# Kernel tuning notes

Measured on AMD Instinct MI355X. Metric: run time of the kernel, lower is better.

## Reference

```python
import jax, jax.numpy as jnp
import numpy as np
from jax import lax

DIM = 512
DH = 16          # dim_head
H = DIM // DH    # 32 heads
WS = 7           # window_size
SR = 3           # sr_ratio (AvgPool2d kernel, stride=1)
EPS = 1e-5


def _rel_pos_indices():
    # mirrors the torch buffer construction, incl. the [:, 24:] slice for sr_ratio>1
    pos = np.arange(WS)
    gi, gj = np.meshgrid(pos, pos, indexing='ij')
    grid = np.stack([gi, gj], axis=-1).reshape(-1, 2)            # (49, 2)
    rel = grid[:, None, :] - grid[None, :, :] + (WS - 1)         # (49, 49, 2)
    idx = rel[..., 0] * (2 * WS - 1) + rel[..., 1]               # (49, 49)
    return jnp.asarray(idx[:, 24:], dtype=jnp.int32)             # (49, 25)


def _layernorm(x, g, b):
    m = jnp.mean(x, axis=-1, keepdims=True)
    v = jnp.mean(jnp.square(x - m), axis=-1, keepdims=True)
    return (x - m) * lax.rsqrt(v + EPS) * g + b


def setup_inputs() -> dict:
    key = jax.random.key(0)
    ks = jax.random.split(key, 8)
    B, X, Y = 8, 14, 14
    x = jax.random.normal(ks[0], (B, X, Y, WS, WS, DIM), dtype=jnp.float32)
    ln_gamma = 1.0 + 0.1 * jax.random.normal(ks[1], (DIM,), dtype=jnp.float32)
    ln_beta = 0.1 * jax.random.normal(ks[2], (DIM,), dtype=jnp.float32)
    s = 1.0 / np.sqrt(DIM)
    Wq = jax.random.normal(ks[3], (DIM, DIM), dtype=jnp.float32) * s
    Wkv = jax.random.normal(ks[4], (2 * DIM, DIM), dtype=jnp.float32) * s
    Wout = jax.random.normal(ks[5], (DIM, DIM), dtype=jnp.float32) * s
    rel_pos_emb = 0.02 * jax.random.normal(ks[6], ((2 * WS - 1) ** 2, H), dtype=jnp.float32)
    return {"x": x, "ln_gamma": ln_gamma, "ln_beta": ln_beta,
            "Wq": Wq, "Wkv": Wkv, "Wout": Wout, "rel_pos_emb": rel_pos_emb}


def reference(x, ln_gamma, ln_beta, Wq, Wkv, Wout, rel_pos_emb):
    B, X, Y, W1, W2, D = x.shape
    Nw = B * X * Y                      # number of windows
    Nq = W1 * W2                        # 49 query tokens per window
    xn = _layernorm(x, ln_gamma, ln_beta)
    xw = xn.reshape(Nw, Nq, D)
    # queries
    q = (xw @ Wq.T).reshape(Nw, Nq, H, DH).transpose(0, 2, 1, 3) * (DH ** -0.5)  # (Nw,H,Nq,DH)
    # KV spatial reduction: AvgPool2d(kernel=SR, stride=1) over the 7x7 window
    xi = xw.reshape(Nw, W1, W2, D)
    xp = lax.reduce_window(xi, 0.0, lax.add, (1, SR, SR, 1), (1, 1, 1, 1), 'VALID') / (SR * SR)
    Hp, Wp = W1 - SR + 1, W2 - SR + 1   # 5, 5
    xkv = _layernorm(xp.reshape(Nw, Hp * Wp, D), ln_gamma, ln_beta)
    # to_kv with einops '(dim h l)' decomposition: last axis factored as (DH, H, 2)
    kv = (xkv @ Wkv.T).reshape(Nw, Hp * Wp, DH, H, 2)
    k = kv[..., 0].transpose(0, 3, 1, 2)  # (Nw, H, Nk, DH)
    v = kv[..., 1].transpose(0, 3, 1, 2)
    sim = jnp.einsum('bhid,bhjd->bhij', q, k)                    # (Nw,H,49,25)
    bias = rel_pos_emb[_rel_pos_indices()]                       # (49,25,H)
    sim = sim + bias.transpose(2, 0, 1)[None]
    attn = jax.nn.softmax(sim, axis=-1)
    out = jnp.einsum('bhij,bhjd->bhid', attn, v)                 # (Nw,H,49,DH)
    out = out.reshape(Nw, H, W1, W2, DH).transpose(0, 2, 3, 1, 4).reshape(Nw, W1, W2, D)
    out = out @ Wout.T
    return out.reshape(B, X, Y, W1, W2, D)
```

## Files before the change

kernel.cpp:

```cpp
#include <hip/hip_runtime.h>

typedef _Float16 half8 __attribute__((ext_vector_type(8)));
typedef float f32x4 __attribute__((ext_vector_type(4)));

#define MFMA16(a,b,c) __builtin_amdgcn_mfma_f32_16x16x32_f16(a,b,c,0,0,0)
#define GLOAD16(g, l) __builtin_amdgcn_global_load_lds( \
  (const __attribute__((address_space(1))) void*)(g), \
  (__attribute__((address_space(3))) void*)(l), 16, 0, 0)

static constexpr int NW     = 1568;
static constexpr int MROWSQ = 76832;
static constexpr int MPADQ  = 76928;
static constexpr int MROWKV = 39200;
static constexpr int MPADKV = 39296;

__device__ __forceinline__ half8 h8z(){
  half8 z = {(_Float16)0,(_Float16)0,(_Float16)0,(_Float16)0,
             (_Float16)0,(_Float16)0,(_Float16)0,(_Float16)0};
  return z;
}

__global__ void k_prep_w(const float* __restrict__ a, const float* __restrict__ b,
                         const float* __restrict__ c,
                         _Float16* __restrict__ ah, _Float16* __restrict__ bh,
                         _Float16* __restrict__ ch){
  int i = blockIdx.x*256 + threadIdx.x;
  if(i < 262144) ah[i] = (_Float16)(a[i]*0.25f);
  int j = i - 262144;
  if(j >= 0 && j < 524288) bh[j] = (_Float16)b[j];
  int k = i - 786432;
  if(k >= 0 && k < 262144) ch[k] = (_Float16)c[k];
}

__global__ void k_prep_bias(const float* __restrict__ rel, float* __restrict__ biasT){
  int t = blockIdx.x*256 + threadIdx.x;
  if(t >= 65536) return;
  int h = t >> 11;
  int r = t & 2047;
  int i = r >> 5, slotk = r & 31;
  int kg = slotk >> 3, idx = slotk & 7;
  int j = (idx < 4) ? (kg*4 + idx) : (16 + kg*4 + idx - 4);
  float v = 0.f;
  if(j >= 25) v = -1e30f;
  else if(i < 49){
    int qi = i/7, qj = i%7;
    int c = j + 24, ki = c/7, kj = c%7;
    v = rel[((qi-ki+6)*13 + (qj-kj+6))*32 + h];
  }
  biasT[t] = v;
}

__global__ __launch_bounds__(512) void k_ln_pool(const float* __restrict__ x,
    const float* __restrict__ gamma, const float* __restrict__ beta,
    _Float16* __restrict__ xn, _Float16* __restrict__ xkv){
  __shared__ _Float16 nrm[49*512];
  const int w = blockIdx.x, t = threadIdx.x;
  const int lane = t & 63, wv = t >> 6;
  float gf[8], bf[8];
  {
    float4 g0 = *(const float4*)(gamma + lane*8);
    float4 g1 = *(const float4*)(gamma + lane*8 + 4);
    float4 b0 = *(const float4*)(beta  + lane*8);
    float4 b1 = *(const float4*)(beta  + lane*8 + 4);
    gf[0]=g0.x; gf[1]=g0.y; gf[2]=g0.z; gf[3]=g0.w;
    gf[4]=g1.x; gf[5]=g1.y; gf[6]=g1.z; gf[7]=g1.w;
    bf[0]=b0.x; bf[1]=b0.y; bf[2]=b0.z; bf[3]=b0.w;
    bf[4]=b1.x; bf[5]=b1.y; bf[6]=b1.z; bf[7]=b1.w;
  }
  const float* xw = x + (size_t)w*49*512;
  for(int i = wv; i < 49; i += 8){
    const float* row = xw + i*512 + lane*8;
    float4 v0 = *(const float4*)row;
    float4 v1 = *(const float4*)(row+4);
    float v[8] = {v0.x,v0.y,v0.z,v0.w,v1.x,v1.y,v1.z,v1.w};
    float s = 0.f, sq = 0.f;
    #pragma unroll
    for(int j=0;j<8;j++){ s += v[j]; sq += v[j]*v[j]; }
    #pragma unroll
    for(int o=32;o>=1;o>>=1){ s += __shfl_xor(s,o); sq += __shfl_xor(sq,o); }
    float mean = s*(1.f/512.f);
    float rstd = rsqrtf(sq*(1.f/512.f) - mean*mean + 1e-5f);
    half8 nh;
    #pragma unroll
    for(int j=0;j<8;j++)
      nh[j] = (_Float16)((v[j]-mean)*rstd*gf[j] + bf[j]);
    *(half8*)&nrm[i*512 + lane*8] = nh;
    *(half8*)(xn + ((size_t)w*49 + i)*512 + lane*8) = nh;
  }
  __syncthreads();
  for(int p = wv; p < 25; p += 8){
    const int pi = p/5, pj = p%5;
    float acc[8] = {0,0,0,0,0,0,0,0};
    #pragma unroll
    for(int a=0;a<3;a++)
      #pragma unroll
      for(int bb=0;bb<3;bb++){
        half8 rv = *(const half8*)&nrm[((pi+a)*7 + (pj+bb))*512 + lane*8];
        #pragma unroll
        for(int j=0;j<8;j++) acc[j] += (float)rv[j];
      }
    float s = 0.f, sq = 0.f;
    #pragma unroll
    for(int j=0;j<8;j++){ acc[j] *= (1.f/9.f); s += acc[j]; sq += acc[j]*acc[j]; }
    #pragma unroll
    for(int o=32;o>=1;o>>=1){ s += __shfl_xor(s,o); sq += __shfl_xor(sq,o); }
    float mean = s*(1.f/512.f);
    float rstd = rsqrtf(sq*(1.f/512.f) - mean*mean + 1e-5f);
    half8 nh;
    #pragma unroll
    for(int j=0;j<8;j++) nh[j] = (_Float16)((acc[j]-mean)*rstd*gf[j] + bf[j]);
    *(half8*)(xkv + ((size_t)w*25 + p)*512 + lane*8) = nh;
  }
}

template<int MODE>
__global__ __launch_bounds__(256) void k_gemm(const _Float16* __restrict__ A,
    const _Float16* __restrict__ Bw, _Float16* __restrict__ oh,
    float* __restrict__ of, int ldc){
  __shared__ __align__(16) _Float16 As[128*32];
  __shared__ __align__(16) _Float16 Bs[128*32];
  const int m0 = blockIdx.y*128, n0 = blockIdx.x*128;
  const int t = threadIdx.x, lane = t & 63;
  const int wid = t >> 6, wm = (wid>>1)*64, wn = (wid&1)*64;
  const int lr = lane & 15, kg = lane >> 4;
  f32x4 acc[4][4] = {};
  const _Float16* Ab = A  + (size_t)m0*512;
  const _Float16* Bb = Bw + (size_t)n0*512;
  for(int k0 = 0; k0 < 512; k0 += 32){
    #pragma unroll
    for(int c=0;c<2;c++){
      int foff = c*256 + wid*64;
      int f = foff + lane;
      const _Float16* sa = Ab + (size_t)(f>>2)*512 + k0 + (f&3)*8;
      const _Float16* sb = Bb + (size_t)(f>>2)*512 + k0 + (f&3)*8;
      GLOAD16(sa, As + foff*8);
      GLOAD16(sb, Bs + foff*8);
    }
    __syncthreads();
    half8 af[4], bf[4];
    #pragma unroll
    for(int mt=0;mt<4;mt++) af[mt] = *(const half8*)&As[(wm + mt*16 + lr)*32 + kg*8];
    #pragma unroll
    for(int nt=0;nt<4;nt++) bf[nt] = *(const half8*)&Bs[(wn + nt*16 + lr)*32 + kg*8];
    #pragma unroll
    for(int mt=0;mt<4;mt++)
      #pragma unroll
      for(int nt=0;nt<4;nt++)
        acc[mt][nt] = MFMA16(af[mt], bf[nt], acc[mt][nt]);
    __syncthreads();
  }
  #pragma unroll
  for(int mt=0;mt<4;mt++)
    #pragma unroll
    for(int nt=0;nt<4;nt++)
      #pragma unroll
      for(int r=0;r<4;r++){
        int row = m0 + wm + mt*16 + kg*4 + r;
        int col = n0 + wn + nt*16 + lr;
        float vv = acc[mt][nt][r];
        if(MODE == 0){
          oh[(size_t)row*ldc + col] = (_Float16)vv;
        } else {
          if(row < MROWSQ) of[(size_t)row*ldc + col] = vv;
        }
      }
}

__global__ __launch_bounds__(256) void k_repack(const _Float16* __restrict__ kvb,
    _Float16* __restrict__ kb, _Float16* __restrict__ vb){
  __shared__ uint2 s2[6400];
  uint32_t* su = (uint32_t*)s2;
  const int w = blockIdx.x, t = threadIdx.x;
  const uint2* src = (const uint2*)(kvb + (size_t)w*25*1024);
  #pragma unroll
  for(int it=0; it<25; ++it){
    int U = it*256 + t;
    int j = U >> 8, u = U & 255;
    s2[j*256 + (u ^ (u>>4) ^ (j&15))] = src[U];
  }
  __syncthreads();
  _Float16* kdst = kb + (size_t)w*12800;
  _Float16* vdst = vb + (size_t)w*12800;
  for(int it=0; it<7; ++it){
    int q = it*256 + t;
    if(q < 1600){
      int h = q/50, rem = q%50, j = rem>>1, half = rem&1;
      half8 k8, v8;
      #pragma unroll
      for(int jj=0;jj<8;jj++){
        int dh = half*8 + jj;
        int slot = j*256 + ((dh*16 + (h>>1)) ^ dh ^ (j&15));
        uint32_t val = su[slot*2 + (h&1)];
        k8[jj] = ((_Float16*)&val)[0];
        v8[jj] = ((_Float16*)&val)[1];
      }
      *(half8*)(kdst + q*8) = k8;
      *(half8*)(vdst + q*8) = v8;
    }
  }
}

__global__ __launch_bounds__(256) void k_attn(const _Float16* __restrict__ q,
    const _Float16* __restrict__ kb, const _Float16* __restrict__ vb,
    const float* __restrict__ biasT, _Float16* __restrict__ ao){
  const int w = blockIdx.x, hi = blockIdx.y, t = threadIdx.x;
  const int lane = t & 63, wv = t >> 6;
  const int lr = lane & 15, kg = lane >> 4;
  const size_t qbase = ((size_t)w*49)*512;
  const int hA = hi*4 + wv;
  const size_t kvA = (((size_t)w*32 + hA)*25)*16;
  const size_t kvB = kvA + 6400;
  half8 kA0=h8z(), kA1=h8z(), kB0=h8z(), kB1=h8z();
  if(kg < 2){
    kA0 = *(const half8*)(kb + kvA + lr*16 + kg*8);
    kB0 = *(const half8*)(kb + kvB + lr*16 + kg*8);
    if(lr < 9){
      kA1 = *(const half8*)(kb + kvA + (16+lr)*16 + kg*8);
      kB1 = *(const half8*)(kb + kvB + (16+lr)*16 + kg*8);
    }
  }
  half8 qA[4], qB[4];
  #pragma unroll
  for(int qt=0;qt<4;qt++){
    if(kg < 2){
      const _Float16* p = q + qbase + (size_t)(qt*16+lr)*512 + hA*16 + kg*8;
      qA[qt] = *(const half8*)p;
      qB[qt] = *(const half8*)(p + 256);
    } else { qA[qt] = h8z(); qB[qt] = h8z(); }
  }
  half8 vA = h8z(), vB = h8z();
  #pragma unroll
  for(int idx=0; idx<8; idx++){
    int key = (idx<4) ? (kg*4+idx) : (16 + kg*4 + idx-4);
    if(key < 25){
      vA[idx] = vb[kvA + key*16 + lr];
      vB[idx] = vb[kvB + key*16 + lr];
    }
  }
  const float4* btA = (const float4*)(biasT + (size_t)hA*2048);
  const float4* btB = (const float4*)(biasT + (size_t)(hA+16)*2048);
  #pragma unroll
  for(int qt=0;qt<4;qt++){
    f32x4 sA0={}, sA1={}, sB0={}, sB1={};
    sA0 = MFMA16(kA0, qA[qt], sA0);
    sA1 = MFMA16(kA1, qA[qt], sA1);
    sB0 = MFMA16(kB0, qB[qt], sB0);
    sB1 = MFMA16(kB1, qB[qt], sB1);
    const int i = qt*16 + lr;
    const int bidx = i*8 + kg*2;
    float4 bA0 = btA[bidx], bA1 = btA[bidx+1];
    float4 bB0 = btB[bidx], bB1 = btB[bidx+1];
    float a[8], b[8];
    a[0]=sA0[0]+bA0.x; a[1]=sA0[1]+bA0.y; a[2]=sA0[2]+bA0.z; a[3]=sA0[3]+bA0.w;
    a[4]=sA1[0]+bA1.x; a[5]=sA1[1]+bA1.y; a[6]=sA1[2]+bA1.z; a[7]=sA1[3]+bA1.w;
    b[0]=sB0[0]+bB0.x; b[1]=sB0[1]+bB0.y; b[2]=sB0[2]+bB0.z; b[3]=sB0[3]+bB0.w;
    b[4]=sB1[0]+bB1.x; b[5]=sB1[1]+bB1.y; b[6]=sB1[2]+bB1.z; b[7]=sB1[3]+bB1.w;
    float mA = a[0], mB = b[0];
    #pragma unroll
    for(int j=1;j<8;j++){ mA = fmaxf(mA, a[j]); mB = fmaxf(mB, b[j]); }
    mA = fmaxf(mA, __shfl_xor(mA,16)); mB = fmaxf(mB, __shfl_xor(mB,16));
    mA = fmaxf(mA, __shfl_xor(mA,32)); mB = fmaxf(mB, __shfl_xor(mB,32));
    float sumA = 0.f, sumB = 0.f;
    #pragma unroll
    for(int j=0;j<8;j++){
      a[j] = __expf(a[j]-mA); sumA += a[j];
      b[j] = __expf(b[j]-mB); sumB += b[j];
    }
    sumA += __shfl_xor(sumA,16); sumB += __shfl_xor(sumB,16);
    sumA += __shfl_xor(sumA,32); sumB += __shfl_xor(sumB,32);
    float invA = 1.f/sumA, invB = 1.f/sumB;
    half8 pA, pB;
    #pragma unroll
    for(int j=0;j<8;j++){
      pA[j] = (_Float16)(a[j]*invA);
      pB[j] = (_Float16)(b[j]*invB);
    }
    f32x4 oA={}, oB={};
    oA = MFMA16(pA, vA, oA);
    oB = MFMA16(pB, vB, oB);
    #pragma unroll
    for(int r=0;r<4;r++){
      int qi2 = qt*16 + kg*4 + r;
      if(qi2 < 49){
        _Float16* dst = ao + qbase + (size_t)qi2*512 + hA*16 + lr;
        dst[0]   = (_Float16)oA[r];
        dst[256] = (_Float16)oB[r];
      }
    }
  }
}

extern "C" void kernel_launch(void* const* d_in, const int* in_sizes, int n_in,
                              void* d_out, int out_size, void* d_ws, size_t ws_size,
                              hipStream_t stream){
  (void)in_sizes; (void)n_in; (void)out_size; (void)ws_size;
  const float* x    = (const float*)d_in[0];
  const float* gam  = (const float*)d_in[1];
  const float* bet  = (const float*)d_in[2];
  const float* Wq   = (const float*)d_in[3];
  const float* Wkv  = (const float*)d_in[4];
  const float* Wout = (const float*)d_in[5];
  const float* rel  = (const float*)d_in[6];
  float* out = (float*)d_out;

  char* ws = (char*)d_ws;
  size_t off = 0;
  auto alloc = [&](size_t n){ char* p = ws + off; off += (n + 1023) & ~(size_t)1023; return p; };
  _Float16* xn    = (_Float16*)alloc((size_t)MPADQ*512*2);
  _Float16* xkv   = (_Float16*)alloc((size_t)MPADKV*512*2);
  _Float16* kvb   = (_Float16*)alloc((size_t)MPADKV*1024*2);
  _Float16* kbuf  = (_Float16*)alloc((size_t)NW*32*25*16*2);
  _Float16* vbuf  = (_Float16*)alloc((size_t)NW*32*25*16*2);
  _Float16* wqh   = (_Float16*)alloc((size_t)262144*2);
  _Float16* wkvh  = (_Float16*)alloc((size_t)524288*2);
  _Float16* wouth = (_Float16*)alloc((size_t)262144*2);
  float*    biasT = (float*)   alloc((size_t)65536*4);
  _Float16* qb    = kvb;

  k_prep_w   <<<dim3(4096), 256, 0, stream>>>(Wq, Wkv, Wout, wqh, wkvh, wouth);
  k_prep_bias<<<dim3(256),  256, 0, stream>>>(rel, biasT);
  k_ln_pool  <<<dim3(NW),   512, 0, stream>>>(x, gam, bet, xn, xkv);
  k_gemm<0>  <<<dim3(8,307),256, 0, stream>>>(xkv, wkvh,  kvb, nullptr, 1024);
  k_repack   <<<dim3(NW),   256, 0, stream>>>(kvb, kbuf, vbuf);
  k_gemm<0>  <<<dim3(4,601),256, 0, stream>>>(xn,  wqh,   qb,  nullptr, 512);
  k_attn     <<<dim3(NW,4), 256, 0, stream>>>(qb, kbuf, vbuf, biasT, xn);
  k_gemm<1>  <<<dim3(4,601),256, 0, stream>>>(xn,  wouth, nullptr, out, 512);
}
```

Before: 407.2 us.

## Double-buffer GEMM LDS tiles and remap blocks across XCDs

The GEMM kernel now uses two LDS buffers so global-to-LDS loads for the next K tile are issued while MFMAs run on the current tile, cutting one barrier per iteration. It also switches to a 1D grid and remaps block IDs so each XCD processes a contiguous range of tiles, which improves L2 reuse of the A rows and weight columns. This doubles LDS use per block, which may lower occupancy.

```diff
diff --git a/kernel.cpp b/kernel.cpp
--- a/kernel.cpp
+++ b/kernel.cpp
@@ -116,38 +116,53 @@
 template<int MODE>
 __global__ __launch_bounds__(256) void k_gemm(const _Float16* __restrict__ A,
     const _Float16* __restrict__ Bw, _Float16* __restrict__ oh,
-    float* __restrict__ of, int ldc){
-  __shared__ __align__(16) _Float16 As[128*32];
-  __shared__ __align__(16) _Float16 Bs[128*32];
-  const int m0 = blockIdx.y*128, n0 = blockIdx.x*128;
+    float* __restrict__ of, int ldc, int ntn, int nwg){
+  __shared__ __align__(16) _Float16 As[2][128*32];
+  __shared__ __align__(16) _Float16 Bs[2][128*32];
+  const int orig = blockIdx.x;
+  const int xcd = orig & 7, slot = orig >> 3;
+  const int q8 = nwg >> 3, r8 = nwg & 7;
+  const int base = (xcd < r8) ? xcd*(q8+1) : r8*(q8+1) + (xcd-r8)*q8;
+  const int lin = base + slot;
+  const int m0 = (lin / ntn) * 128, n0 = (lin % ntn) * 128;
   const int t = threadIdx.x, lane = t & 63;
   const int wid = t >> 6, wm = (wid>>1)*64, wn = (wid&1)*64;
   const int lr = lane & 15, kg = lane >> 4;
-  f32x4 acc[4][4] = {};
   const _Float16* Ab = A  + (size_t)m0*512;
   const _Float16* Bb = Bw + (size_t)n0*512;
-  for(int k0 = 0; k0 < 512; k0 += 32){
-    #pragma unroll
-    for(int c=0;c<2;c++){
-      int foff = c*256 + wid*64;
-      int f = foff + lane;
-      const _Float16* sa = Ab + (size_t)(f>>2)*512 + k0 + (f&3)*8;
-      const _Float16* sb = Bb + (size_t)(f>>2)*512 + k0 + (f&3)*8;
-      GLOAD16(sa, As + foff*8);
-      GLOAD16(sb, Bs + foff*8);
-    }
-    __syncthreads();
+  const int foff0 = wid*64, foff1 = 256 + wid*64;
+  const int f0 = foff0 + lane, f1 = foff1 + lane;
+  const size_t ga0 = (size_t)(f0>>2)*512 + (f0&3)*8;
+  const size_t ga1 = (size_t)(f1>>2)*512 + (f1&3)*8;
+
+  GLOAD16(Ab + ga0, &As[0][foff0*8]);
+  GLOAD16(Bb + ga0, &Bs[0][foff0*8]);
+  GLOAD16(Ab + ga1, &As[0][foff1*8]);
+  GLOAD16(Bb + ga1, &Bs[0][foff1*8]);
+  __syncthreads();
+
+  f32x4 acc[4][4] = {};
+  int cur = 0;
+  for(int kt = 0; kt < 16; ++kt){
+    if(kt < 15){
+      const int k0 = (kt+1)*32;
+      GLOAD16(Ab + ga0 + k0, &As[cur^1][foff0*8]);
+      GLOAD16(Bb + ga0 + k0, &Bs[cur^1][foff0*8]);
+      GLOAD16(Ab + ga1 + k0, &As[cur^1][foff1*8]);
+      GLOAD16(Bb + ga1 + k0, &Bs[cur^1][foff1*8]);
+    }
     half8 af[4], bf[4];
     #pragma unroll
-    for(int mt=0;mt<4;mt++) af[mt] = *(const half8*)&As[(wm + mt*16 + lr)*32 + kg*8];
-    #pragma unroll
-    for(int nt=0;nt<4;nt++) bf[nt] = *(const half8*)&Bs[(wn + nt*16 + lr)*32 + kg*8];
+    for(int mt=0;mt<4;mt++) af[mt] = *(const half8*)&As[cur][(wm + mt*16 + lr)*32 + kg*8];
+    #pragma unroll
+    for(int nt=0;nt<4;nt++) bf[nt] = *(const half8*)&Bs[cur][(wn + nt*16 + lr)*32 + kg*8];
     #pragma unroll
     for(int mt=0;mt<4;mt++)
       #pragma unroll
       for(int nt=0;nt<4;nt++)
         acc[mt][nt] = MFMA16(af[mt], bf[nt], acc[mt][nt]);
     __syncthreads();
+    cur ^= 1;
   }
   #pragma unroll
   for(int mt=0;mt<4;mt++)
@@ -320,9 +335,9 @@
   k_prep_w   <<<dim3(4096), 256, 0, stream>>>(Wq, Wkv, Wout, wqh, wkvh, wouth);
   k_prep_bias<<<dim3(256),  256, 0, stream>>>(rel, biasT);
   k_ln_pool  <<<dim3(NW),   512, 0, stream>>>(x, gam, bet, xn, xkv);
-  k_gemm<0>  <<<dim3(8,307),256, 0, stream>>>(xkv, wkvh,  kvb, nullptr, 1024);
+  k_gemm<0>  <<<dim3(2456), 256, 0, stream>>>(xkv, wkvh,  kvb, nullptr, 1024, 8, 2456);
   k_repack   <<<dim3(NW),   256, 0, stream>>>(kvb, kbuf, vbuf);
-  k_gemm<0>  <<<dim3(4,601),256, 0, stream>>>(xn,  wqh,   qb,  nullptr, 512);
+  k_gemm<0>  <<<dim3(2404), 256, 0, stream>>>(xn,  wqh,   qb,  nullptr,  512, 4, 2404);
   k_attn     <<<dim3(NW,4), 256, 0, stream>>>(qb, kbuf, vbuf, biasT, xn);
-  k_gemm<1>  <<<dim3(4,601),256, 0, stream>>>(xn,  wouth, nullptr, out, 512);
-}
+  k_gemm<1>  <<<dim3(2404), 256, 0, stream>>>(xn,  wouth, nullptr, out,  512, 4, 2404);
+}
```

After: 396.2 us. 2.7% less time.
